# Kernel tuning notes

Hardware: AMD Instinct MI355X
Metric: run time of the kernel (lower is better)

The kernel has to match this reference:

```python
import jax, jax.numpy as jnp
import numpy as np

B, T, IN, H, OUT = 512, 1000, 39, 64, 48


def setup_inputs() -> dict:
    key = jax.random.key(0)
    ks = jax.random.split(key, 7)
    s = 1.0 / np.sqrt(H)
    return {
        "x": jax.random.normal(ks[0], (B, T, IN), dtype=jnp.float32),
        "W_ih": jax.random.uniform(ks[1], (4 * H, IN), minval=-s, maxval=s, dtype=jnp.float32),
        "W_hh": jax.random.uniform(ks[2], (4 * H, H), minval=-s, maxval=s, dtype=jnp.float32),
        "b_ih": jax.random.uniform(ks[3], (4 * H,), minval=-s, maxval=s, dtype=jnp.float32),
        "b_hh": jax.random.uniform(ks[4], (4 * H,), minval=-s, maxval=s, dtype=jnp.float32),
        "W_out": jax.random.uniform(ks[5], (OUT, H), minval=-s, maxval=s, dtype=jnp.float32),
        "b_out": jax.random.uniform(ks[6], (OUT,), minval=-s, maxval=s, dtype=jnp.float32),
    }


def reference(x, W_ih, W_hh, b_ih, b_hh, W_out, b_out):
    # Single-layer batch-first LSTM (zero init state) + per-step Linear + sigmoid.
    b = b_ih + b_hh  # [4H]
    # Precompute input projections for all timesteps at once: [T, B, 4H]
    xg = jnp.einsum('bti,gi->tbg', x, W_ih) + b

    def step(carry, xg_t):
        h, c = carry
        gates = xg_t + h @ W_hh.T  # [B, 4H], gate order i, f, g, o
        i, f, g, o = jnp.split(gates, 4, axis=-1)
        c = jax.nn.sigmoid(f) * c + jax.nn.sigmoid(i) * jnp.tanh(g)
        h = jax.nn.sigmoid(o) * jnp.tanh(c)
        y = jax.nn.sigmoid(h @ W_out.T + b_out)  # [B, OUT]
        return (h, c), y

    h0 = jnp.zeros((x.shape[0], W_hh.shape[1]), dtype=x.dtype)
    (_, _), ys = jax.lax.scan(step, (h0, h0), xg)  # ys: [T, B, OUT]
    return jnp.swapaxes(ys, 0, 1)  # [B, T, OUT]
```

## Files before the change

### kernel.cpp

```cpp
#include <hip/hip_runtime.h>


#define BB 512
#define TT 1000
#define INF 39
#define HH 64
#define OUTF 48
#define G4 (4 * HH)

#define Q10(M) M(0) M(1) M(2) M(3) M(4) M(5) M(6) M(7) M(8) M(9)
#define Q16(M) M(0) M(1) M(2) M(3) M(4) M(5) M(6) M(7) \
               M(8) M(9) M(10) M(11) M(12) M(13) M(14) M(15)

__global__ __launch_bounds__(256, 2) void lstm_fused_kernel(
    const float* __restrict__ x,
    const float* __restrict__ W_ih,
    const float* __restrict__ W_hh,
    const float* __restrict__ b_ih,
    const float* __restrict__ b_hh,
    const float* __restrict__ W_out,
    const float* __restrict__ b_out,
    float* __restrict__ out)
{
    const int b = blockIdx.x;
    const int tid = threadIdx.x;

    __shared__ float xs[40];
    __shared__ float hs[HH];
    __shared__ float act[G4];

    const float* wih_ptr = W_ih + tid * INF;
#define LOAD_IH4(q) float4 wiq##q; \
    wiq##q.x = wih_ptr[4*(q)]; \
    wiq##q.y = (4*(q)+1 < INF) ? wih_ptr[4*(q)+1] : 0.f; \
    wiq##q.z = (4*(q)+2 < INF) ? wih_ptr[4*(q)+2] : 0.f; \
    wiq##q.w = (4*(q)+3 < INF) ? wih_ptr[4*(q)+3] : 0.f;
    Q10(LOAD_IH4)

    const float4* wh4p = (const float4*)(W_hh + tid * HH);
#define LOAD_HH4(i) const float4 wh##i = wh4p[i];
    Q16(LOAD_HH4)

    const float bias = b_ih[tid] + b_hh[tid];

    const int o = tid >> 2;
    const int p = tid & 3;
    float4 wo0, wo1, wo2, wo3;
    float bo = 0.f;
    if (tid < 4 * OUTF) {
        const float4* wop = (const float4*)(W_out + o * HH + p * 16);
        wo0 = wop[0]; wo1 = wop[1]; wo2 = wop[2]; wo3 = wop[3];
        bo = b_out[o];
    } else {
        wo0 = wo1 = wo2 = wo3 = make_float4(0.f, 0.f, 0.f, 0.f);
    }

    float c = 0.f;
    const size_t x_base = (size_t)b * TT * INF;
    const size_t out_base = (size_t)b * TT * OUTF;

    if (tid < HH) hs[tid] = 0.f;
    if (tid < INF) xs[tid] = x[x_base + tid];
    if (tid == 39) xs[39] = 0.f;
    float xreg = (tid < INF) ? x[x_base + INF + tid] : 0.f;

    const int gate_type = tid >> 6;
    __syncthreads();

    const float4* xs4 = (const float4*)xs;
    const float4* hs4 = (const float4*)hs;

    for (int t = 0; t < TT; ++t) {
        float a0 = bias, a1 = 0.f, a2 = 0.f, a3 = 0.f;
#define FMA_IH4(q) { const float4 xv = xs4[q]; \
        a0 += xv.x * wiq##q.x; a1 += xv.y * wiq##q.y; \
        a2 += xv.z * wiq##q.z; a3 += xv.w * wiq##q.w; }
        Q10(FMA_IH4)
#define FMA_HH4(i) { const float4 hv = hs4[i]; \
        a0 += hv.x * wh##i.x; a1 += hv.y * wh##i.y; \
        a2 += hv.z * wh##i.z; a3 += hv.w * wh##i.w; }
        Q16(FMA_HH4)
        const float acc = (a0 + a1) + (a2 + a3);

        float a;
        if (gate_type == 2) {
            a = 2.f / (1.f + __expf(-2.f * acc)) - 1.f;
        } else {
            a = 1.f / (1.f + __expf(-acc));
        }
        act[tid] = a;
        __syncthreads();

        if (tid < INF) {
            xs[tid] = xreg;
            if (t + 2 < TT) xreg = x[x_base + (size_t)(t + 2) * INF + tid];
        }
        if (tid < HH) {
            const float ig = act[tid];
            const float fg = act[HH + tid];
            const float gg = act[2 * HH + tid];
            const float og = act[3 * HH + tid];
            c = fg * c + ig * gg;
            const float th = 2.f / (1.f + __expf(-2.f * c)) - 1.f;
            hs[tid] = og * th;
        }
        __syncthreads();

        if (tid < 4 * OUTF) {
            const float4 h0 = hs4[p * 4 + 0];
            const float4 h1 = hs4[p * 4 + 1];
            const float4 h2 = hs4[p * 4 + 2];
            const float4 h3 = hs4[p * 4 + 3];
            float s0 = h0.x * wo0.x + h0.y * wo0.y + h0.z * wo0.z + h0.w * wo0.w;
            float s1 = h1.x * wo1.x + h1.y * wo1.y + h1.z * wo1.z + h1.w * wo1.w;
            float s2 = h2.x * wo2.x + h2.y * wo2.y + h2.z * wo2.z + h2.w * wo2.w;
            float s3 = h3.x * wo3.x + h3.y * wo3.y + h3.z * wo3.z + h3.w * wo3.w;
            float s = (s0 + s1) + (s2 + s3);
            s += __shfl_xor(s, 1, 64);
            s += __shfl_xor(s, 2, 64);
            if (p == 0) {
                const float y = 1.f / (1.f + __expf(-(s + bo)));
                __builtin_nontemporal_store(y, &out[out_base + (size_t)t * OUTF + o]);
            }
        }
    }
}

extern "C" void kernel_launch(void* const* d_in, const int* in_sizes, int n_in,
                              void* d_out, int out_size, void* d_ws, size_t ws_size,
                              hipStream_t stream) {
    const float* x     = (const float*)d_in[0];
    const float* W_ih  = (const float*)d_in[1];
    const float* W_hh  = (const float*)d_in[2];
    const float* b_ih  = (const float*)d_in[3];
    const float* b_hh  = (const float*)d_in[4];
    const float* W_out = (const float*)d_in[5];
    const float* b_out = (const float*)d_in[6];
    float* out = (float*)d_out;

    lstm_fused_kernel<<<dim3(BB), dim3(G4), 0, stream>>>(
        x, W_ih, W_hh, b_ih, b_hh, W_out, b_out, out);
}
```

Before: 1.076 ms.

## Split LSTM into producer and recurrent waves with packed FMA and double buffering

Restructures the kernel into two wavefronts per batch element. One wave precomputes the input projection for step t+1 and the output projection for step t-1 into double-buffered shared memory. The other wave keeps all four gates' W_hh rows in registers per hidden unit and runs the recurrence using packed v2f FMAs, so each step needs one barrier instead of two and no shared gate-activation exchange. The cost is very high register pressure in the recurrent wave and a serial critical path of about 128 packed FMAs per lane per step. Each block now has fewer waves (two instead of four), so there is less parallelism available to hide latency.

```diff
diff --git a/kernel.cpp b/kernel.cpp
--- a/kernel.cpp
+++ b/kernel.cpp
@@ -6,122 +6,171 @@
 #define INF 39
 #define HH 64
 #define OUTF 48
-#define G4 (4 * HH)
+
+typedef float v2f __attribute__((ext_vector_type(2)));
 
 #define Q10(M) M(0) M(1) M(2) M(3) M(4) M(5) M(6) M(7) M(8) M(9)
 #define Q16(M) M(0) M(1) M(2) M(3) M(4) M(5) M(6) M(7) \
                M(8) M(9) M(10) M(11) M(12) M(13) M(14) M(15)
 
-__global__ __launch_bounds__(256, 2) void lstm_fused_kernel(
-    const float* __restrict__ x,
-    const float* __restrict__ W_ih,
-    const float* __restrict__ W_hh,
-    const float* __restrict__ b_ih,
-    const float* __restrict__ b_hh,
-    const float* __restrict__ W_out,
-    const float* __restrict__ b_out,
-    float* __restrict__ out)
+__global__ __launch_bounds__(128, 1)
+void lstm_pc_kernel(const float* __restrict__ x,
+                    const float* __restrict__ W_ih,
+                    const float* __restrict__ W_hh,
+                    const float* __restrict__ b_ih,
+                    const float* __restrict__ b_hh,
+                    const float* __restrict__ W_out,
+                    const float* __restrict__ b_out,
+                    float* __restrict__ out)
 {
-    const int b = blockIdx.x;
-    const int tid = threadIdx.x;
+    const int b    = blockIdx.x;
+    const int lane = threadIdx.x & 63;
+    const int wav  = threadIdx.x >> 6;
 
     __shared__ float xs[40];
-    __shared__ float hs[HH];
-    __shared__ float act[G4];
+    __shared__ float xgb[2][4 * HH];
+    __shared__ float hsb[2][HH];
 
-    const float* wih_ptr = W_ih + tid * INF;
-#define LOAD_IH4(q) float4 wiq##q; \
-    wiq##q.x = wih_ptr[4*(q)]; \
-    wiq##q.y = (4*(q)+1 < INF) ? wih_ptr[4*(q)+1] : 0.f; \
-    wiq##q.z = (4*(q)+2 < INF) ? wih_ptr[4*(q)+2] : 0.f; \
-    wiq##q.w = (4*(q)+3 < INF) ? wih_ptr[4*(q)+3] : 0.f;
-    Q10(LOAD_IH4)
-
-    const float4* wh4p = (const float4*)(W_hh + tid * HH);
-#define LOAD_HH4(i) const float4 wh##i = wh4p[i];
-    Q16(LOAD_HH4)
-
-    const float bias = b_ih[tid] + b_hh[tid];
-
-    const int o = tid >> 2;
-    const int p = tid & 3;
-    float4 wo0, wo1, wo2, wo3;
-    float bo = 0.f;
-    if (tid < 4 * OUTF) {
-        const float4* wop = (const float4*)(W_out + o * HH + p * 16);
-        wo0 = wop[0]; wo1 = wop[1]; wo2 = wop[2]; wo3 = wop[3];
-        bo = b_out[o];
-    } else {
-        wo0 = wo1 = wo2 = wo3 = make_float4(0.f, 0.f, 0.f, 0.f);
-    }
-
-    float c = 0.f;
-    const size_t x_base = (size_t)b * TT * INF;
+    const size_t x_base   = (size_t)b * TT * INF;
     const size_t out_base = (size_t)b * TT * OUTF;
 
-    if (tid < HH) hs[tid] = 0.f;
-    if (tid < INF) xs[tid] = x[x_base + tid];
-    if (tid == 39) xs[39] = 0.f;
-    float xreg = (tid < INF) ? x[x_base + INF + tid] : 0.f;
+    if (wav == 1) {
+        const int m = lane;
 
-    const int gate_type = tid >> 6;
-    __syncthreads();
+#define LIH(g, q) v2f wiA##g##_##q, wiB##g##_##q; { \
+        const float* wp_ = W_ih + ((g) * HH + m) * INF; \
+        wiA##g##_##q.x = wp_[4*(q)]; \
+        wiA##g##_##q.y = (4*(q)+1 < INF) ? wp_[4*(q)+1] : 0.f; \
+        wiB##g##_##q.x = (4*(q)+2 < INF) ? wp_[4*(q)+2] : 0.f; \
+        wiB##g##_##q.y = (4*(q)+3 < INF) ? wp_[4*(q)+3] : 0.f; }
+#define LIH0(q) LIH(0, q)
+#define LIH1(q) LIH(1, q)
+#define LIH2(q) LIH(2, q)
+#define LIH3(q) LIH(3, q)
+        Q10(LIH0) Q10(LIH1) Q10(LIH2) Q10(LIH3)
 
-    const float4* xs4 = (const float4*)xs;
-    const float4* hs4 = (const float4*)hs;
+        const float bg0 = b_ih[0*HH+m] + b_hh[0*HH+m];
+        const float bg1 = b_ih[1*HH+m] + b_hh[1*HH+m];
+        const float bg2 = b_ih[2*HH+m] + b_hh[2*HH+m];
+        const float bg3 = b_ih[3*HH+m] + b_hh[3*HH+m];
 
-    for (int t = 0; t < TT; ++t) {
-        float a0 = bias, a1 = 0.f, a2 = 0.f, a3 = 0.f;
-#define FMA_IH4(q) { const float4 xv = xs4[q]; \
-        a0 += xv.x * wiq##q.x; a1 += xv.y * wiq##q.y; \
-        a2 += xv.z * wiq##q.z; a3 += xv.w * wiq##q.w; }
-        Q10(FMA_IH4)
-#define FMA_HH4(i) { const float4 hv = hs4[i]; \
-        a0 += hv.x * wh##i.x; a1 += hv.y * wh##i.y; \
-        a2 += hv.z * wh##i.z; a3 += hv.w * wh##i.w; }
-        Q16(FMA_HH4)
-        const float acc = (a0 + a1) + (a2 + a3);
+#define DWO(k) v2f woA##k = {0.f, 0.f}, woB##k = {0.f, 0.f};
+        Q16(DWO)
+        float bo = 0.f;
+        if (m < OUTF) {
+            const float4* wp_ = (const float4*)(W_out + m * HH);
+#define LWO(k) { const float4 q_ = wp_[k]; \
+            woA##k = (v2f){q_.x, q_.y}; woB##k = (v2f){q_.z, q_.w}; }
+            Q16(LWO)
+            bo = b_out[m];
+        }
 
-        float a;
-        if (gate_type == 2) {
-            a = 2.f / (1.f + __expf(-2.f * acc)) - 1.f;
-        } else {
-            a = 1.f / (1.f + __expf(-acc));
-        }
-        act[tid] = a;
+#define XQ(q) { const float4 xq_ = xs4_[q]; \
+        const v2f xA_ = {xq_.x, xq_.y}, xB_ = {xq_.z, xq_.w}; \
+        a0A += xA_ * wiA0_##q; a0B += xB_ * wiB0_##q; \
+        a1A += xA_ * wiA1_##q; a1B += xB_ * wiB1_##q; \
+        a2A += xA_ * wiA2_##q; a2B += xB_ * wiB2_##q; \
+        a3A += xA_ * wiA3_##q; a3B += xB_ * wiB3_##q; }
+
+#define XG_COMPUTE(BUF) { \
+        const float4* xs4_ = (const float4*)xs; \
+        v2f a0A = {bg0, 0.f}, a0B = {0.f, 0.f}; \
+        v2f a1A = {bg1, 0.f}, a1B = {0.f, 0.f}; \
+        v2f a2A = {bg2, 0.f}, a2B = {0.f, 0.f}; \
+        v2f a3A = {bg3, 0.f}, a3B = {0.f, 0.f}; \
+        Q10(XQ) \
+        xgb[BUF][0*HH+m] = (a0A.x+a0A.y)+(a0B.x+a0B.y); \
+        xgb[BUF][1*HH+m] = (a1A.x+a1A.y)+(a1B.x+a1B.y); \
+        xgb[BUF][2*HH+m] = (a2A.x+a2A.y)+(a2B.x+a2B.y); \
+        xgb[BUF][3*HH+m] = (a3A.x+a3A.y)+(a3B.x+a3B.y); }
+
+#define OQ(k) { const float4 hq_ = hv_[k]; \
+        sA += (v2f){hq_.x, hq_.y} * woA##k; \
+        sB += (v2f){hq_.z, hq_.w} * woB##k; }
+
+#define OUTPROJ(TIDX) { \
+        const float4* hv_ = (const float4*)hsb[(TIDX) & 1]; \
+        v2f sA = {0.f, 0.f}, sB = {0.f, 0.f}; \
+        Q16(OQ) \
+        if (m < OUTF) { \
+            const float s_ = (sA.x+sA.y)+(sB.x+sB.y) + bo; \
+            const float y_ = 1.f / (1.f + __expf(-s_)); \
+            __builtin_nontemporal_store(y_, \
+                &out[out_base + (size_t)(TIDX) * OUTF + m]); } }
+
+        if (m < INF)  xs[m]   = x[x_base + m];
+        if (m == INF) xs[INF] = 0.f;
+        float xreg = (m < INF) ? x[x_base + INF + m] : 0.f;
+        XG_COMPUTE(0)
         __syncthreads();
 
-        if (tid < INF) {
-            xs[tid] = xreg;
-            if (t + 2 < TT) xreg = x[x_base + (size_t)(t + 2) * INF + tid];
+        for (int t = 0; t < TT; ++t) {
+            if (t + 1 < TT) {
+                if (m < INF) {
+                    xs[m] = xreg;
+                    if (t + 2 < TT) xreg = x[x_base + (size_t)(t + 2) * INF + m];
+                }
+            }
+            if (t >= 1) OUTPROJ(t - 1)
+            if (t + 1 < TT) XG_COMPUTE((t + 1) & 1)
+            __syncthreads();
         }
-        if (tid < HH) {
-            const float ig = act[tid];
-            const float fg = act[HH + tid];
-            const float gg = act[2 * HH + tid];
-            const float og = act[3 * HH + tid];
-            c = fg * c + ig * gg;
-            const float th = 2.f / (1.f + __expf(-2.f * c)) - 1.f;
-            hs[tid] = og * th;
-        }
+        OUTPROJ(TT - 1)
+
+    } else {
+#define LHH(g, k) v2f whA##g##_##k, whB##g##_##k; { \
+        const float4 q_ = ((const float4*)(W_hh + ((g)*HH + lane) * HH))[k]; \
+        whA##g##_##k = (v2f){q_.x, q_.y}; whB##g##_##k = (v2f){q_.z, q_.w}; }
+#define LHH0(k) LHH(0, k)
+#define LHH1(k) LHH(1, k)
+#define LHH2(k) LHH(2, k)
+#define LHH3(k) LHH(3, k)
+        Q16(LHH0) Q16(LHH1) Q16(LHH2) Q16(LHH3)
+
+#define DNH(k) float4 nh##k = make_float4(0.f, 0.f, 0.f, 0.f);
+        Q16(DNH)
+
+        float c = 0.f;
         __syncthreads();
 
-        if (tid < 4 * OUTF) {
-            const float4 h0 = hs4[p * 4 + 0];
-            const float4 h1 = hs4[p * 4 + 1];
-            const float4 h2 = hs4[p * 4 + 2];
-            const float4 h3 = hs4[p * 4 + 3];
-            float s0 = h0.x * wo0.x + h0.y * wo0.y + h0.z * wo0.z + h0.w * wo0.w;
-            float s1 = h1.x * wo1.x + h1.y * wo1.y + h1.z * wo1.z + h1.w * wo1.w;
-            float s2 = h2.x * wo2.x + h2.y * wo2.y + h2.z * wo2.z + h2.w * wo2.w;
-            float s3 = h3.x * wo3.x + h3.y * wo3.y + h3.z * wo3.z + h3.w * wo3.w;
-            float s = (s0 + s1) + (s2 + s3);
-            s += __shfl_xor(s, 1, 64);
-            s += __shfl_xor(s, 2, 64);
-            if (p == 0) {
-                const float y = 1.f / (1.f + __expf(-(s + bo)));
-                __builtin_nontemporal_store(y, &out[out_base + (size_t)t * OUTF + o]);
-            }
+#define HQ(k) { const v2f hA_ = {nh##k.x, nh##k.y}, hB_ = {nh##k.z, nh##k.w}; \
+        a0A += hA_ * whA0_##k; a0B += hB_ * whB0_##k; \
+        a1A += hA_ * whA1_##k; a1B += hB_ * whB1_##k; \
+        a2A += hA_ * whA2_##k; a2B += hB_ * whB2_##k; \
+        a3A += hA_ * whA3_##k; a3B += hB_ * whB3_##k; }
+
+        for (int t = 0; t < TT; ++t) {
+            const int cb = t & 1;
+            const float xg0_ = xgb[cb][0*HH + lane];
+            const float xg1_ = xgb[cb][1*HH + lane];
+            const float xg2_ = xgb[cb][2*HH + lane];
+            const float xg3_ = xgb[cb][3*HH + lane];
+
+            v2f a0A = {0.f,0.f}, a0B = {0.f,0.f};
+            v2f a1A = {0.f,0.f}, a1B = {0.f,0.f};
+            v2f a2A = {0.f,0.f}, a2B = {0.f,0.f};
+            v2f a3A = {0.f,0.f}, a3B = {0.f,0.f};
+            Q16(HQ)
+
+            const float pi_ = (a0A.x+a0A.y)+(a0B.x+a0B.y) + xg0_;
+            const float pf_ = (a1A.x+a1A.y)+(a1B.x+a1B.y) + xg1_;
+            const float pg_ = (a2A.x+a2A.y)+(a2B.x+a2B.y) + xg2_;
+            const float po_ = (a3A.x+a3A.y)+(a3B.x+a3B.y) + xg3_;
+
+            const float si = 1.f / (1.f + __expf(-pi_));
+            const float sf = 1.f / (1.f + __expf(-pf_));
+            const float tg = 2.f / (1.f + __expf(-2.f * pg_)) - 1.f;
+            const float so = 1.f / (1.f + __expf(-po_));
+
+            c = fmaf(sf, c, si * tg);
+            const float th = 2.f / (1.f + __expf(-2.f * c)) - 1.f;
+            const float hN = so * th;
+
+            hsb[cb][lane] = hN;
+            const float4* hv_ = (const float4*)hsb[cb];
+#define RNH(k) nh##k = hv_[k];
+            Q16(RNH)
+            __syncthreads();
         }
     }
 }
@@ -138,6 +187,6 @@
     const float* b_out = (const float*)d_in[6];
     float* out = (float*)d_out;
 
-    lstm_fused_kernel<<<dim3(BB), dim3(G4), 0, stream>>>(
+    lstm_pc_kernel<<<dim3(BB), dim3(128), 0, stream>>>(
         x, W_ih, W_hh, b_ih, b_hh, W_out, b_out, out);
 }
```

Result: faster. 967.1 us (-10.2%).

## Split LSTM gate reduction over K across waves, pipeline output projection

Applied to the files above, without the earlier changes.

Work is repartitioned so each wave owns a 16-wide slice of the hidden dimension (and a 10-wide slice of the input) for all four gates of its lane, producing partial sums that wave 0 reduces and turns into the cell update. The output projection for step t-1 is computed from the same h slice in the same pass, which removes one barrier phase per timestep. Packed two-wide float FMAs are used for the dot products. This cuts the per-step serial chain from three barrier phases to two, in exchange for extra shared-memory partial-sum traffic and a final reduction done by a single wave.

```diff
diff --git a/kernel.cpp b/kernel.cpp
--- a/kernel.cpp
+++ b/kernel.cpp
@@ -6,122 +6,175 @@
 #define INF 39
 #define HH 64
 #define OUTF 48
-#define G4 (4 * HH)
 
-#define Q10(M) M(0) M(1) M(2) M(3) M(4) M(5) M(6) M(7) M(8) M(9)
-#define Q16(M) M(0) M(1) M(2) M(3) M(4) M(5) M(6) M(7) \
-               M(8) M(9) M(10) M(11) M(12) M(13) M(14) M(15)
+typedef float v2f __attribute__((ext_vector_type(2)));
 
-__global__ __launch_bounds__(256, 2) void lstm_fused_kernel(
-    const float* __restrict__ x,
-    const float* __restrict__ W_ih,
-    const float* __restrict__ W_hh,
-    const float* __restrict__ b_ih,
-    const float* __restrict__ b_hh,
-    const float* __restrict__ W_out,
-    const float* __restrict__ b_out,
-    float* __restrict__ out)
+__device__ __forceinline__ float sigf(float v) { return 1.f / (1.f + __expf(-v)); }
+__device__ __forceinline__ float tanhx(float v) { return 2.f / (1.f + __expf(-2.f * v)) - 1.f; }
+
+__global__ __launch_bounds__(256, 2)
+void lstm_splitk(const float* __restrict__ x,
+                 const float* __restrict__ W_ih,
+                 const float* __restrict__ W_hh,
+                 const float* __restrict__ b_ih,
+                 const float* __restrict__ b_hh,
+                 const float* __restrict__ W_out,
+                 const float* __restrict__ b_out,
+                 float* __restrict__ out)
 {
-    const int b = blockIdx.x;
-    const int tid = threadIdx.x;
+    const int b    = blockIdx.x;
+    const int lane = threadIdx.x & 63;
+    const int wav  = threadIdx.x >> 6;
+    const int K0   = wav * 16;
+    const int I0   = wav * 10;
 
-    __shared__ float xs[40];
-    __shared__ float hs[HH];
-    __shared__ float act[G4];
+    __shared__ float  xs[40];
+    __shared__ float  hs[HH];
+    __shared__ float4 parts[4][64];
+    __shared__ float  yp[4][OUTF];
 
-    const float* wih_ptr = W_ih + tid * INF;
-#define LOAD_IH4(q) float4 wiq##q; \
-    wiq##q.x = wih_ptr[4*(q)]; \
-    wiq##q.y = (4*(q)+1 < INF) ? wih_ptr[4*(q)+1] : 0.f; \
-    wiq##q.z = (4*(q)+2 < INF) ? wih_ptr[4*(q)+2] : 0.f; \
-    wiq##q.w = (4*(q)+3 < INF) ? wih_ptr[4*(q)+3] : 0.f;
-    Q10(LOAD_IH4)
+    const size_t x_base   = (size_t)b * TT * INF;
+    const size_t out_base = (size_t)b * TT * OUTF;
 
-    const float4* wh4p = (const float4*)(W_hh + tid * HH);
-#define LOAD_HH4(i) const float4 wh##i = wh4p[i];
-    Q16(LOAD_HH4)
-
-    const float bias = b_ih[tid] + b_hh[tid];
-
-    const int o = tid >> 2;
-    const int p = tid & 3;
-    float4 wo0, wo1, wo2, wo3;
-    float bo = 0.f;
-    if (tid < 4 * OUTF) {
-        const float4* wop = (const float4*)(W_out + o * HH + p * 16);
-        wo0 = wop[0]; wo1 = wop[1]; wo2 = wop[2]; wo3 = wop[3];
-        bo = b_out[o];
-    } else {
-        wo0 = wo1 = wo2 = wo3 = make_float4(0.f, 0.f, 0.f, 0.f);
+    float4 wh[4][4];
+#pragma unroll
+    for (int g = 0; g < 4; ++g) {
+        const float4* p = (const float4*)(W_hh + (g * HH + lane) * HH + K0);
+        wh[g][0] = p[0]; wh[g][1] = p[1]; wh[g][2] = p[2]; wh[g][3] = p[3];
     }
 
+    float wi[4][10];
+#pragma unroll
+    for (int g = 0; g < 4; ++g) {
+        const float* p = W_ih + (g * HH + lane) * INF;
+#pragma unroll
+        for (int j = 0; j < 10; ++j) {
+            const int i = I0 + j;
+            wi[g][j] = (i < INF) ? p[i] : 0.f;
+        }
+    }
+
+    float4 wo[4];
+    wo[0] = wo[1] = wo[2] = wo[3] = make_float4(0.f, 0.f, 0.f, 0.f);
+    float bo = 0.f;
+    if (lane < OUTF) {
+        const float4* p = (const float4*)(W_out + lane * HH + K0);
+        wo[0] = p[0]; wo[1] = p[1]; wo[2] = p[2]; wo[3] = p[3];
+        bo = b_out[lane];
+    }
+
+    float bg[4];
+#pragma unroll
+    for (int g = 0; g < 4; ++g) bg[g] = b_ih[g * HH + lane] + b_hh[g * HH + lane];
+
+    if (wav == 0) hs[lane] = 0.f;
+    if (wav == 2) {
+        if (lane < INF) xs[lane] = x[x_base + lane];
+        if (lane == INF) xs[INF] = 0.f;
+    }
+    float xreg = (wav == 2 && lane < INF) ? x[x_base + INF + lane] : 0.f;
     float c = 0.f;
-    const size_t x_base = (size_t)b * TT * INF;
-    const size_t out_base = (size_t)b * TT * OUTF;
-
-    if (tid < HH) hs[tid] = 0.f;
-    if (tid < INF) xs[tid] = x[x_base + tid];
-    if (tid == 39) xs[39] = 0.f;
-    float xreg = (tid < INF) ? x[x_base + INF + tid] : 0.f;
-
-    const int gate_type = tid >> 6;
     __syncthreads();
 
-    const float4* xs4 = (const float4*)xs;
-    const float4* hs4 = (const float4*)hs;
+    for (int t = 0; t < TT; ++t) {
+        const float4* hs4 = (const float4*)hs;
+        const float4 hq0 = hs4[wav * 4 + 0];
+        const float4 hq1 = hs4[wav * 4 + 1];
+        const float4 hq2 = hs4[wav * 4 + 2];
+        const float4 hq3 = hs4[wav * 4 + 3];
 
-    for (int t = 0; t < TT; ++t) {
-        float a0 = bias, a1 = 0.f, a2 = 0.f, a3 = 0.f;
-#define FMA_IH4(q) { const float4 xv = xs4[q]; \
-        a0 += xv.x * wiq##q.x; a1 += xv.y * wiq##q.y; \
-        a2 += xv.z * wiq##q.z; a3 += xv.w * wiq##q.w; }
-        Q10(FMA_IH4)
-#define FMA_HH4(i) { const float4 hv = hs4[i]; \
-        a0 += hv.x * wh##i.x; a1 += hv.y * wh##i.y; \
-        a2 += hv.z * wh##i.z; a3 += hv.w * wh##i.w; }
-        Q16(FMA_HH4)
-        const float acc = (a0 + a1) + (a2 + a3);
+        float xv[10];
+#pragma unroll
+        for (int j = 0; j < 10; ++j) xv[j] = xs[I0 + j];
 
-        float a;
-        if (gate_type == 2) {
-            a = 2.f / (1.f + __expf(-2.f * acc)) - 1.f;
-        } else {
-            a = 1.f / (1.f + __expf(-acc));
+        float sg_[4];
+#pragma unroll
+        for (int g = 0; g < 4; ++g) {
+            v2f aA = { (wav == 0) ? bg[g] : 0.f, 0.f };
+            v2f aB = { 0.f, 0.f };
+            aA += (v2f){hq0.x, hq0.y} * (v2f){wh[g][0].x, wh[g][0].y};
+            aB += (v2f){hq0.z, hq0.w} * (v2f){wh[g][0].z, wh[g][0].w};
+            aA += (v2f){hq1.x, hq1.y} * (v2f){wh[g][1].x, wh[g][1].y};
+            aB += (v2f){hq1.z, hq1.w} * (v2f){wh[g][1].z, wh[g][1].w};
+            aA += (v2f){hq2.x, hq2.y} * (v2f){wh[g][2].x, wh[g][2].y};
+            aB += (v2f){hq2.z, hq2.w} * (v2f){wh[g][2].z, wh[g][2].w};
+            aA += (v2f){hq3.x, hq3.y} * (v2f){wh[g][3].x, wh[g][3].y};
+            aB += (v2f){hq3.z, hq3.w} * (v2f){wh[g][3].z, wh[g][3].w};
+            aA += (v2f){xv[0], xv[1]} * (v2f){wi[g][0], wi[g][1]};
+            aB += (v2f){xv[2], xv[3]} * (v2f){wi[g][2], wi[g][3]};
+            aA += (v2f){xv[4], xv[5]} * (v2f){wi[g][4], wi[g][5]};
+            aB += (v2f){xv[6], xv[7]} * (v2f){wi[g][6], wi[g][7]};
+            aA += (v2f){xv[8], xv[9]} * (v2f){wi[g][8], wi[g][9]};
+            sg_[g] = (aA.x + aA.y) + (aB.x + aB.y);
         }
-        act[tid] = a;
+
+        float yv;
+        {
+            v2f yA = {0.f, 0.f}, yB = {0.f, 0.f};
+            yA += (v2f){hq0.x, hq0.y} * (v2f){wo[0].x, wo[0].y};
+            yB += (v2f){hq0.z, hq0.w} * (v2f){wo[0].z, wo[0].w};
+            yA += (v2f){hq1.x, hq1.y} * (v2f){wo[1].x, wo[1].y};
+            yB += (v2f){hq1.z, hq1.w} * (v2f){wo[1].z, wo[1].w};
+            yA += (v2f){hq2.x, hq2.y} * (v2f){wo[2].x, wo[2].y};
+            yB += (v2f){hq2.z, hq2.w} * (v2f){wo[2].z, wo[2].w};
+            yA += (v2f){hq3.x, hq3.y} * (v2f){wo[3].x, wo[3].y};
+            yB += (v2f){hq3.z, hq3.w} * (v2f){wo[3].z, wo[3].w};
+            yv = (yA.x + yA.y) + (yB.x + yB.y);
+        }
+
+        if (wav != 0) parts[wav][lane] = make_float4(sg_[0], sg_[1], sg_[2], sg_[3]);
+        if (wav != 1 && lane < OUTF) yp[wav][lane] = yv;
         __syncthreads();
 
-        if (tid < INF) {
-            xs[tid] = xreg;
-            if (t + 2 < TT) xreg = x[x_base + (size_t)(t + 2) * INF + tid];
-        }
-        if (tid < HH) {
-            const float ig = act[tid];
-            const float fg = act[HH + tid];
-            const float gg = act[2 * HH + tid];
-            const float og = act[3 * HH + tid];
-            c = fg * c + ig * gg;
-            const float th = 2.f / (1.f + __expf(-2.f * c)) - 1.f;
-            hs[tid] = og * th;
+        if (wav == 0) {
+            const float4 p1 = parts[1][lane];
+            const float4 p2 = parts[2][lane];
+            const float4 p3 = parts[3][lane];
+            const float gi = sg_[0] + p1.x + p2.x + p3.x;
+            const float gf = sg_[1] + p1.y + p2.y + p3.y;
+            const float gg = sg_[2] + p1.z + p2.z + p3.z;
+            const float go = sg_[3] + p1.w + p2.w + p3.w;
+            const float si = sigf(gi);
+            const float sf = sigf(gf);
+            const float tg = tanhx(gg);
+            const float so = sigf(go);
+            c = fmaf(sf, c, si * tg);
+            hs[lane] = so * tanhx(c);
+        } else if (wav == 1) {
+            if (t >= 1 && lane < OUTF) {
+                const float y = sigf(yv + yp[0][lane] + yp[2][lane] + yp[3][lane] + bo);
+                __builtin_nontemporal_store(y, &out[out_base + (size_t)(t - 1) * OUTF + lane]);
+            }
+        } else if (wav == 2) {
+            if (lane < INF) {
+                xs[lane] = xreg;
+                if (t + 2 < TT) xreg = x[x_base + (size_t)(t + 2) * INF + lane];
+            }
         }
         __syncthreads();
+    }
 
-        if (tid < 4 * OUTF) {
-            const float4 h0 = hs4[p * 4 + 0];
-            const float4 h1 = hs4[p * 4 + 1];
-            const float4 h2 = hs4[p * 4 + 2];
-            const float4 h3 = hs4[p * 4 + 3];
-            float s0 = h0.x * wo0.x + h0.y * wo0.y + h0.z * wo0.z + h0.w * wo0.w;
-            float s1 = h1.x * wo1.x + h1.y * wo1.y + h1.z * wo1.z + h1.w * wo1.w;
-            float s2 = h2.x * wo2.x + h2.y * wo2.y + h2.z * wo2.z + h2.w * wo2.w;
-            float s3 = h3.x * wo3.x + h3.y * wo3.y + h3.z * wo3.z + h3.w * wo3.w;
-            float s = (s0 + s1) + (s2 + s3);
-            s += __shfl_xor(s, 1, 64);
-            s += __shfl_xor(s, 2, 64);
-            if (p == 0) {
-                const float y = 1.f / (1.f + __expf(-(s + bo)));
-                __builtin_nontemporal_store(y, &out[out_base + (size_t)t * OUTF + o]);
-            }
+    {
+        const float4* hs4 = (const float4*)hs;
+        const float4 hq0 = hs4[wav * 4 + 0];
+        const float4 hq1 = hs4[wav * 4 + 1];
+        const float4 hq2 = hs4[wav * 4 + 2];
+        const float4 hq3 = hs4[wav * 4 + 3];
+        v2f yA = {0.f, 0.f}, yB = {0.f, 0.f};
+        yA += (v2f){hq0.x, hq0.y} * (v2f){wo[0].x, wo[0].y};
+        yB += (v2f){hq0.z, hq0.w} * (v2f){wo[0].z, wo[0].w};
+        yA += (v2f){hq1.x, hq1.y} * (v2f){wo[1].x, wo[1].y};
+        yB += (v2f){hq1.z, hq1.w} * (v2f){wo[1].z, wo[1].w};
+        yA += (v2f){hq2.x, hq2.y} * (v2f){wo[2].x, wo[2].y};
+        yB += (v2f){hq2.z, hq2.w} * (v2f){wo[2].z, wo[2].w};
+        yA += (v2f){hq3.x, hq3.y} * (v2f){wo[3].x, wo[3].y};
+        yB += (v2f){hq3.z, hq3.w} * (v2f){wo[3].z, wo[3].w};
+        const float yvv = (yA.x + yA.y) + (yB.x + yB.y);
+        if (wav != 1 && lane < OUTF) yp[wav][lane] = yvv;
+        __syncthreads();
+        if (wav == 1 && lane < OUTF) {
+            const float y = sigf(yvv + yp[0][lane] + yp[2][lane] + yp[3][lane] + bo);
+            __builtin_nontemporal_store(y, &out[out_base + (size_t)(TT - 1) * OUTF + lane]);
         }
     }
 }
@@ -138,6 +191,6 @@
     const float* b_out = (const float*)d_in[6];
     float* out = (float*)d_out;
 
-    lstm_fused_kernel<<<dim3(BB), dim3(G4), 0, stream>>>(
+    lstm_splitk<<<dim3(BB), dim3(256), 0, stream>>>(
         x, W_ih, W_hh, b_ih, b_hh, W_out, b_out, out);
 }
```

After: 871.7 us. 1.23x faster.

## Process two sequences per block with LDS-resident weights and K-split gate reduction

Applied to the files above, without the earlier changes.

Each block now handles two batch sequences. Gate weights move from registers into shared memory in a gate-interleaved float4 layout, and the recurrent and input dot products are split across the four waves by K. Partial sums are reduced through shared memory, and one wave per sequence applies the cell update. The output projection for step t-1 is fused into the step-t pass over h, which removes one barrier per step. Packed v2f math is used throughout. In exchange there is more LDS traffic per step, higher LDS usage per block, and half as many blocks.

```diff
diff --git a/kernel.cpp b/kernel.cpp
--- a/kernel.cpp
+++ b/kernel.cpp
@@ -6,122 +6,191 @@
 #define INF 39
 #define HH 64
 #define OUTF 48
-#define G4 (4 * HH)
-
-#define Q10(M) M(0) M(1) M(2) M(3) M(4) M(5) M(6) M(7) M(8) M(9)
-#define Q16(M) M(0) M(1) M(2) M(3) M(4) M(5) M(6) M(7) \
-               M(8) M(9) M(10) M(11) M(12) M(13) M(14) M(15)
-
-__global__ __launch_bounds__(256, 2) void lstm_fused_kernel(
-    const float* __restrict__ x,
-    const float* __restrict__ W_ih,
-    const float* __restrict__ W_hh,
-    const float* __restrict__ b_ih,
-    const float* __restrict__ b_hh,
-    const float* __restrict__ W_out,
-    const float* __restrict__ b_out,
-    float* __restrict__ out)
+
+typedef float v2f __attribute__((ext_vector_type(2)));
+
+__device__ __forceinline__ float sigf(float v)  { return 1.f / (1.f + __expf(-v)); }
+__device__ __forceinline__ float tanhx(float v) { return 2.f / (1.f + __expf(-2.f * v)) - 1.f; }
+
+__global__ __launch_bounds__(256, 1)
+void lstm_ldsk(const float* __restrict__ x,
+               const float* __restrict__ W_ih,
+               const float* __restrict__ W_hh,
+               const float* __restrict__ b_ih,
+               const float* __restrict__ b_hh,
+               const float* __restrict__ W_out,
+               const float* __restrict__ b_out,
+               float* __restrict__ out)
 {
-    const int b = blockIdx.x;
     const int tid = threadIdx.x;
-
-    __shared__ float xs[40];
-    __shared__ float hs[HH];
-    __shared__ float act[G4];
-
-    const float* wih_ptr = W_ih + tid * INF;
-#define LOAD_IH4(q) float4 wiq##q; \
-    wiq##q.x = wih_ptr[4*(q)]; \
-    wiq##q.y = (4*(q)+1 < INF) ? wih_ptr[4*(q)+1] : 0.f; \
-    wiq##q.z = (4*(q)+2 < INF) ? wih_ptr[4*(q)+2] : 0.f; \
-    wiq##q.w = (4*(q)+3 < INF) ? wih_ptr[4*(q)+3] : 0.f;
-    Q10(LOAD_IH4)
-
-    const float4* wh4p = (const float4*)(W_hh + tid * HH);
-#define LOAD_HH4(i) const float4 wh##i = wh4p[i];
-    Q16(LOAD_HH4)
-
-    const float bias = b_ih[tid] + b_hh[tid];
-
-    const int o = tid >> 2;
-    const int p = tid & 3;
-    float4 wo0, wo1, wo2, wo3;
+    const int j   = tid & 63;
+    const int w   = tid >> 6;
+    const int blk = blockIdx.x;
+
+    __shared__ float4 whhG[HH * 64];
+    __shared__ float4 wihG[40 * 64];
+    __shared__ float4 parts[2][4][64];
+    __shared__ float  yparts[2][4][64];
+    __shared__ __align__(16) float hsb[2][2][HH];
+    __shared__ __align__(16) float xsb[2][2][40];
+
+    for (int idx = tid; idx < HH * 64; idx += 256) {
+        const int k = idx >> 6, jj = idx & 63;
+        whhG[idx] = make_float4(W_hh[(0*HH+jj)*HH + k], W_hh[(1*HH+jj)*HH + k],
+                                W_hh[(2*HH+jj)*HH + k], W_hh[(3*HH+jj)*HH + k]);
+    }
+    for (int idx = tid; idx < 40 * 64; idx += 256) {
+        const int i = idx >> 6, jj = idx & 63;
+        float4 v = make_float4(0.f, 0.f, 0.f, 0.f);
+        if (i < INF)
+            v = make_float4(W_ih[(0*HH+jj)*INF + i], W_ih[(1*HH+jj)*INF + i],
+                            W_ih[(2*HH+jj)*INF + i], W_ih[(3*HH+jj)*INF + i]);
+        wihG[idx] = v;
+    }
+
+    float woa[16];
     float bo = 0.f;
-    if (tid < 4 * OUTF) {
-        const float4* wop = (const float4*)(W_out + o * HH + p * 16);
-        wo0 = wop[0]; wo1 = wop[1]; wo2 = wop[2]; wo3 = wop[3];
-        bo = b_out[o];
+    if (j < OUTF) {
+        const float4* p = (const float4*)(W_out + j * HH + 16 * w);
+#pragma unroll
+        for (int q = 0; q < 4; ++q) {
+            const float4 v = p[q];
+            woa[4*q+0] = v.x; woa[4*q+1] = v.y; woa[4*q+2] = v.z; woa[4*q+3] = v.w;
+        }
+        bo = b_out[j];
     } else {
-        wo0 = wo1 = wo2 = wo3 = make_float4(0.f, 0.f, 0.f, 0.f);
-    }
-
+#pragma unroll
+        for (int k = 0; k < 16; ++k) woa[k] = 0.f;
+    }
+
+    const float bg0 = b_ih[0*HH+j] + b_hh[0*HH+j];
+    const float bg1 = b_ih[1*HH+j] + b_hh[1*HH+j];
+    const float bg2 = b_ih[2*HH+j] + b_hh[2*HH+j];
+    const float bg3 = b_ih[3*HH+j] + b_hh[3*HH+j];
+
+    ((float*)hsb)[tid] = 0.f;
+    if (tid < 4) xsb[tid >> 1][tid & 1][39] = 0.f;
+
+    const size_t xbA = (size_t)(2*blk) * TT * INF;
+    const size_t xbB = xbA + (size_t)TT * INF;
+    const size_t obA = (size_t)(2*blk) * TT * OUTF;
+    const size_t obB = obA + (size_t)TT * OUTF;
+
+    float xreg = 0.f;
+    if (w == 2 && j < INF) { xsb[0][0][j] = x[xbA + j]; xreg = x[xbA + INF + j]; }
+    if (w == 3 && j < INF) { xsb[0][1][j] = x[xbB + j]; xreg = x[xbB + INF + j]; }
     float c = 0.f;
-    const size_t x_base = (size_t)b * TT * INF;
-    const size_t out_base = (size_t)b * TT * OUTF;
-
-    if (tid < HH) hs[tid] = 0.f;
-    if (tid < INF) xs[tid] = x[x_base + tid];
-    if (tid == 39) xs[39] = 0.f;
-    float xreg = (tid < INF) ? x[x_base + INF + tid] : 0.f;
-
-    const int gate_type = tid >> 6;
     __syncthreads();
 
-    const float4* xs4 = (const float4*)xs;
-    const float4* hs4 = (const float4*)hs;
+    const int kbase = 16 * w;
+    const float4* wk = whhG + kbase * 64 + j;
+    const float4* wi = wihG + (10 * w) * 64 + j;
 
     for (int t = 0; t < TT; ++t) {
-        float a0 = bias, a1 = 0.f, a2 = 0.f, a3 = 0.f;
-#define FMA_IH4(q) { const float4 xv = xs4[q]; \
-        a0 += xv.x * wiq##q.x; a1 += xv.y * wiq##q.y; \
-        a2 += xv.z * wiq##q.z; a3 += xv.w * wiq##q.w; }
-        Q10(FMA_IH4)
-#define FMA_HH4(i) { const float4 hv = hs4[i]; \
-        a0 += hv.x * wh##i.x; a1 += hv.y * wh##i.y; \
-        a2 += hv.z * wh##i.z; a3 += hv.w * wh##i.w; }
-        Q16(FMA_HH4)
-        const float acc = (a0 + a1) + (a2 + a3);
-
-        float a;
-        if (gate_type == 2) {
-            a = 2.f / (1.f + __expf(-2.f * acc)) - 1.f;
+        const int par = t & 1;
+        const float* hA = hsb[par ^ 1][0];
+        const float* hB = hsb[par ^ 1][1];
+        const float* xA = xsb[par][0];
+        const float* xB = xsb[par][1];
+
+        v2f aA01 = {0.f,0.f}, aA23 = {0.f,0.f};
+        v2f aB01 = {0.f,0.f}, aB23 = {0.f,0.f};
+        v2f yv   = {0.f,0.f};
+
+#define HHK(K) { \
+        const float4 wg = wk[(K) * 64]; \
+        const float ha = hA[kbase + (K)]; \
+        const float hb = hB[kbase + (K)]; \
+        aA01 += (v2f){wg.x, wg.y} * (v2f){ha, ha}; \
+        aA23 += (v2f){wg.z, wg.w} * (v2f){ha, ha}; \
+        aB01 += (v2f){wg.x, wg.y} * (v2f){hb, hb}; \
+        aB23 += (v2f){wg.z, wg.w} * (v2f){hb, hb}; \
+        yv   += (v2f){ha, hb} * (v2f){woa[K], woa[K]}; }
+        HHK(0)  HHK(1)  HHK(2)  HHK(3)  HHK(4)  HHK(5)  HHK(6)  HHK(7)
+        HHK(8)  HHK(9)  HHK(10) HHK(11) HHK(12) HHK(13) HHK(14) HHK(15)
+#undef HHK
+
+#define XIK(I) { \
+        const float4 wg = wi[(I) * 64]; \
+        const float xa = xA[10*w + (I)]; \
+        const float xb = xB[10*w + (I)]; \
+        aA01 += (v2f){wg.x, wg.y} * (v2f){xa, xa}; \
+        aA23 += (v2f){wg.z, wg.w} * (v2f){xa, xa}; \
+        aB01 += (v2f){wg.x, wg.y} * (v2f){xb, xb}; \
+        aB23 += (v2f){wg.z, wg.w} * (v2f){xb, xb}; }
+        XIK(0) XIK(1) XIK(2) XIK(3) XIK(4) XIK(5) XIK(6) XIK(7) XIK(8) XIK(9)
+#undef XIK
+
+        if (w != 0) parts[0][w][j] = make_float4(aA01.x, aA01.y, aA23.x, aA23.y);
+        if (w != 1) parts[1][w][j] = make_float4(aB01.x, aB01.y, aB23.x, aB23.y);
+        if (w != 2) yparts[0][w][j] = yv.x;
+        if (w != 3) yparts[1][w][j] = yv.y;
+        __syncthreads();
+
+        if (w == 0) {
+            const float4 p1 = parts[0][1][j];
+            const float4 p2 = parts[0][2][j];
+            const float4 p3 = parts[0][3][j];
+            const float gi = aA01.x + p1.x + p2.x + p3.x + bg0;
+            const float gf = aA01.y + p1.y + p2.y + p3.y + bg1;
+            const float gg = aA23.x + p1.z + p2.z + p3.z + bg2;
+            const float go = aA23.y + p1.w + p2.w + p3.w + bg3;
+            c = fmaf(sigf(gf), c, sigf(gi) * tanhx(gg));
+            hsb[par][0][j] = sigf(go) * tanhx(c);
+        } else if (w == 1) {
+            const float4 p0 = parts[1][0][j];
+            const float4 p2 = parts[1][2][j];
+            const float4 p3 = parts[1][3][j];
+            const float gi = aB01.x + p0.x + p2.x + p3.x + bg0;
+            const float gf = aB01.y + p0.y + p2.y + p3.y + bg1;
+            const float gg = aB23.x + p0.z + p2.z + p3.z + bg2;
+            const float go = aB23.y + p0.w + p2.w + p3.w + bg3;
+            c = fmaf(sigf(gf), c, sigf(gi) * tanhx(gg));
+            hsb[par][1][j] = sigf(go) * tanhx(c);
+        } else if (w == 2) {
+            if (j < INF) {
+                xsb[par ^ 1][0][j] = xreg;
+                if (t + 2 < TT) xreg = x[xbA + (size_t)(t + 2) * INF + j];
+            }
+            if (t >= 1 && j < OUTF) {
+                const float s = yv.x + yparts[0][0][j] + yparts[0][1][j] + yparts[0][3][j];
+                __builtin_nontemporal_store(sigf(s + bo),
+                    &out[obA + (size_t)(t - 1) * OUTF + j]);
+            }
         } else {
-            a = 1.f / (1.f + __expf(-acc));
-        }
-        act[tid] = a;
+            if (j < INF) {
+                xsb[par ^ 1][1][j] = xreg;
+                if (t + 2 < TT) xreg = x[xbB + (size_t)(t + 2) * INF + j];
+            }
+            if (t >= 1 && j < OUTF) {
+                const float s = yv.y + yparts[1][0][j] + yparts[1][1][j] + yparts[1][2][j];
+                __builtin_nontemporal_store(sigf(s + bo),
+                    &out[obB + (size_t)(t - 1) * OUTF + j]);
+            }
+        }
         __syncthreads();
-
-        if (tid < INF) {
-            xs[tid] = xreg;
-            if (t + 2 < TT) xreg = x[x_base + (size_t)(t + 2) * INF + tid];
-        }
-        if (tid < HH) {
-            const float ig = act[tid];
-            const float fg = act[HH + tid];
-            const float gg = act[2 * HH + tid];
-            const float og = act[3 * HH + tid];
-            c = fg * c + ig * gg;
-            const float th = 2.f / (1.f + __expf(-2.f * c)) - 1.f;
-            hs[tid] = og * th;
-        }
+    }
+
+    {
+        const float* hA = hsb[1][0];
+        const float* hB = hsb[1][1];
+        v2f yv = {0.f, 0.f};
+#define YK(K) yv += (v2f){hA[kbase + (K)], hB[kbase + (K)]} * (v2f){woa[K], woa[K]};
+        YK(0)  YK(1)  YK(2)  YK(3)  YK(4)  YK(5)  YK(6)  YK(7)
+        YK(8)  YK(9)  YK(10) YK(11) YK(12) YK(13) YK(14) YK(15)
+#undef YK
+        if (w != 2) yparts[0][w][j] = yv.x;
+        if (w != 3) yparts[1][w][j] = yv.y;
         __syncthreads();
-
-        if (tid < 4 * OUTF) {
-            const float4 h0 = hs4[p * 4 + 0];
-            const float4 h1 = hs4[p * 4 + 1];
-            const float4 h2 = hs4[p * 4 + 2];
-            const float4 h3 = hs4[p * 4 + 3];
-            float s0 = h0.x * wo0.x + h0.y * wo0.y + h0.z * wo0.z + h0.w * wo0.w;
-            float s1 = h1.x * wo1.x + h1.y * wo1.y + h1.z * wo1.z + h1.w * wo1.w;
-            float s2 = h2.x * wo2.x + h2.y * wo2.y + h2.z * wo2.z + h2.w * wo2.w;
-            float s3 = h3.x * wo3.x + h3.y * wo3.y + h3.z * wo3.z + h3.w * wo3.w;
-            float s = (s0 + s1) + (s2 + s3);
-            s += __shfl_xor(s, 1, 64);
-            s += __shfl_xor(s, 2, 64);
-            if (p == 0) {
-                const float y = 1.f / (1.f + __expf(-(s + bo)));
-                __builtin_nontemporal_store(y, &out[out_base + (size_t)t * OUTF + o]);
-            }
+        if (w == 2 && j < OUTF) {
+            const float s = yv.x + yparts[0][0][j] + yparts[0][1][j] + yparts[0][3][j];
+            __builtin_nontemporal_store(sigf(s + bo),
+                &out[obA + (size_t)(TT - 1) * OUTF + j]);
+        }
+        if (w == 3 && j < OUTF) {
+            const float s = yv.y + yparts[1][0][j] + yparts[1][1][j] + yparts[1][2][j];
+            __builtin_nontemporal_store(sigf(s + bo),
+                &out[obB + (size_t)(TT - 1) * OUTF + j]);
         }
     }
 }
@@ -138,6 +207,6 @@
     const float* b_out = (const float*)d_in[6];
     float* out = (float*)d_out;
 
-    lstm_fused_kernel<<<dim3(BB), dim3(G4), 0, stream>>>(
+    lstm_ldsk<<<dim3(BB / 2), dim3(256), 0, stream>>>(
         x, W_ih, W_hh, b_ih, b_hh, W_out, b_out, out);
 }
```

After: 1.139 ms. 1.06x slower.
